# Kernel tuning notes

Measured on AMD Instinct MI355X. Metric: run time of the kernel, lower is better.

Reference implementation:

```python
import jax, jax.numpy as jnp
import numpy as np

# DynamicMaskHead config (CondLaneHead defaults, head_layers=3, channels=64)
N, INS_PER_IMG, C, H, W = 4, 8, 64, 160, 256
CIN = C + 2  # coords concatenated
L1, L2, L3 = (C + 2) * C, C * C, C * 1  # weight_nums = [4224, 4096, 64]
B1, B2, B3 = C, C, 1                     # bias_nums   = [64, 64, 1]
NUM_PARAMS = L1 + L2 + L3 + B1 + B2 + B3  # 8513
MASK_BIAS_SHIFT = 2.19  # subtracted from last bias when is_mask=True


def setup_inputs() -> dict:
    key = jax.random.key(0)
    k1, k2 = jax.random.split(key)
    x = jax.random.normal(k1, (N, C, H, W), dtype=jnp.float32)
    mask_head_params = jax.random.normal(k2, (N * INS_PER_IMG, NUM_PARAMS), dtype=jnp.float32) * 0.05
    num_ins = np.full((N,), INS_PER_IMG, dtype=np.int32)  # static per-image instance counts
    return {"x": x, "mask_head_params": mask_head_params, "num_ins": num_ins}


def _locations(h, w, dtype):
    # compute_locations with stride=1: +stride//2 == +0; original normalization
    # (locations[:0], locations[:1]) is a no-op slice, so coords stay unnormalized.
    loc_x = jnp.broadcast_to(jnp.arange(w, dtype=dtype)[None, :], (h, w))
    loc_y = jnp.broadcast_to(jnp.arange(h, dtype=dtype)[:, None], (h, w))
    return jnp.stack([loc_x, loc_y], axis=0)  # [2, H, W]


def reference(x, mask_head_params, num_ins):
    n, _, h, w = x.shape
    loc = _locations(h, w, x.dtype)
    xa = jnp.concatenate([jnp.broadcast_to(loc[None], (n, 2, h, w)), x], axis=1)  # [N, 66, H, W]

    # replicate each image's features per instance (grouped-conv input)
    img_idx = np.repeat(np.arange(n), np.asarray(num_ins))  # static
    num_insts = img_idx.shape[0]
    feats = xa[img_idx].reshape(num_insts, CIN, h * w)  # [I, 66, L]

    # parse_dynamic_params: split flat params into per-instance 1x1 conv weights/biases
    splits = jnp.split(mask_head_params, np.cumsum([L1, L2, L3, B1, B2]), axis=1)
    w0 = splits[0].reshape(num_insts, C, CIN)
    w1 = splits[1].reshape(num_insts, C, C)
    w2 = splits[2].reshape(num_insts, 1, C)
    b0 = splits[3]
    b1 = splits[4]
    b2 = splits[5] - MASK_BIAS_SHIFT  # is_mask=True

    # grouped 1x1 convs == per-instance small matmuls (batched GEMM)
    hdn = jax.nn.relu(jnp.einsum('ioc,icl->iol', w0, feats) + b0[:, :, None])
    hdn = jax.nn.relu(jnp.einsum('ioc,icl->iol', w1, hdn) + b1[:, :, None])
    out = jnp.einsum('ioc,icl->iol', w2, hdn) + b2[:, :, None]  # [I, 1, L]
    return out.reshape(1, num_insts, h, w)
```

## Files before the change

kernel.cpp:

```cpp
#include <hip/hip_runtime.h>
#include <hip/hip_bf16.h>


#define NP 8513
#define HW 40960
#define ISTRIDE 18432
#define OFF_VECA 8192
#define OFF_W1 9216
#define OFF_VECB 17408

typedef __attribute__((ext_vector_type(8))) short bf16x8;
typedef __attribute__((ext_vector_type(4))) float f32x4;
typedef __attribute__((ext_vector_type(2))) unsigned uint2v;

__device__ inline unsigned short f2bf(float f) {
  union { float f; unsigned u; } v; v.f = f;
  unsigned r = v.u + 0x7fffu + ((v.u >> 16) & 1u);
  return (unsigned short)(r >> 16);
}
__device__ inline unsigned pk2(float a, float b) {
  __hip_bfloat162 h = __float22bfloat162_rn(float2{a, b});
  union { __hip_bfloat162 h; unsigned u; } v; v.h = h;
  return v.u;
}
__device__ inline void gld16(const void* g, void* l) {
  __builtin_amdgcn_global_load_lds(
      (const __attribute__((address_space(1))) unsigned*)g,
      (__attribute__((address_space(3))) unsigned*)l, 16, 0, 0);
}

__global__ void condlane_prep(const float* __restrict__ params,
                              char* __restrict__ ws) {
  const int inst = blockIdx.x >> 3, part = blockIdx.x & 7;
  const float* __restrict__ p = params + inst * NP;
  char* base = ws + inst * ISTRIDE;
  const int t = threadIdx.x;
  if (part < 4) {
    unsigned short* dst = (unsigned short*)base;
#pragma unroll
    for (int it = 0; it < 4; it++) {
      const int e = (part * 4 + it) * 256 + t;
      const int frag = e >> 9, lane = (e >> 3) & 63, j = e & 7;
      const int m = (frag >> 1) * 16 + (lane & 15);
      const int k = (frag & 1) * 32 + ((lane >> 4) << 3) + j;
      dst[e] = f2bf(p[m * 66 + 2 + k]);
    }
  } else {
    unsigned short* dst = (unsigned short*)(base + OFF_W1);
#pragma unroll
    for (int it = 0; it < 4; it++) {
      const int e = ((part - 4) * 4 + it) * 256 + t;
      const int frag = e >> 9, lane = (e >> 3) & 63, j = e & 7;
      const int m = (frag >> 1) * 16 + (lane & 15);
      const int k = (frag & 1) * 32 + ((lane >> 4) << 3) + j;
      dst[e] = f2bf(p[4224 + m * 64 + k]);
    }
    if (part == 4) {
      float* vA = (float*)(base + OFF_VECA);
      float* vB = (float*)(base + OFF_VECB);
      if (t < 64) {
        vA[t]       = p[8384 + t];
        vA[64 + t]  = p[t * 66];
        vA[128 + t] = p[t * 66 + 1];
        vB[t]       = p[8448 + t];
        vB[64 + t]  = p[8320 + t];
      } else if (t == 64) vB[128] = p[8512] - 2.19f;
    }
  }
}

__global__ __launch_bounds__(256, 3) void condlane_main(
    const float* __restrict__ x, const char* __restrict__ ws,
    float* __restrict__ out) {
  __shared__ __align__(16) char smem[2 * ISTRIDE];
  const int img = blockIdx.y, row = blockIdx.x;
  const int tid = threadIdx.x, lane = tid & 63, wave = tid >> 6;
  const int col = lane & 15, q = lane >> 4;
  const char* const wsb = ws + img * 8 * ISTRIDE;

  auto dma = [&](int i, char* buf) {
    const char* src = wsb + i * ISTRIDE;
#pragma unroll
    for (int u = 0; u < 4; u++) {
      const int off = (wave * 4 + u) * 1024;
      gld16(src + off + lane * 16, buf + off);
    }
    if (wave < 2) {
      const int off = (16 + wave) * 1024;
      gld16(src + off + lane * 16, buf + off);
    }
  };
  dma(0, smem);

  bf16x8 bfr[4][2];
  {
    const float* gx = x + img * 64 * HW + row * 256 + wave * 64;
#pragma unroll
    for (int nt = 0; nt < 4; nt++)
#pragma unroll
      for (int ks = 0; ks < 2; ks++) {
        float f[8];
#pragma unroll
        for (int j = 0; j < 8; j++)
          f[j] = gx[(ks * 32 + q * 8 + j) * HW + nt * 16 + col];
        union { bf16x8 v; unsigned d[4]; } u;
#pragma unroll
        for (int jj = 0; jj < 4; jj++) u.d[jj] = pk2(f[2 * jj], f[2 * jj + 1]);
        bfr[nt][ks] = u.v;
      }
  }
  __syncthreads();

  const float fyv = (float)row;
  float fxv[4];
#pragma unroll
  for (int nt = 0; nt < 4; nt++) fxv[nt] = (float)(wave * 64 + nt * 16 + col);
  float* const outb = out + img * 8 * HW + row * 256 + wave * 64;

  for (int i = 0; i < 8; i++) {
    char* const wb = smem + (i & 1) * ISTRIDE;
    if (i < 7) dma(i + 1, smem + ((i + 1) & 1) * ISTRIDE);
    const float* const vecA = (const float*)(wb + OFF_VECA);
    const float* const vecB = (const float*)(wb + OFF_VECB);

    f32x4 acc[4][4];
#pragma unroll
    for (int mt = 0; mt < 4; mt++) {
      const int ro = mt * 16 + q * 4;
      const f32x4 b0v = *(const f32x4*)(vecA + ro);
      const f32x4 wxv = *(const f32x4*)(vecA + 64 + ro);
      const f32x4 wyv = *(const f32x4*)(vecA + 128 + ro);
      const f32x4 byv = b0v + wyv * fyv;
#pragma unroll
      for (int nt = 0; nt < 4; nt++) acc[mt][nt] = byv + wxv * fxv[nt];
    }
#pragma unroll
    for (int mt = 0; mt < 4; mt++) {
      const bf16x8 a0 = *(const bf16x8*)(wb + (mt * 2 + 0) * 1024 + lane * 16);
      const bf16x8 a1 = *(const bf16x8*)(wb + (mt * 2 + 1) * 1024 + lane * 16);
#pragma unroll
      for (int nt = 0; nt < 4; nt++) {
        f32x4 c = __builtin_amdgcn_mfma_f32_16x16x32_bf16(a0, bfr[nt][0],
                                                          acc[mt][nt], 0, 0, 0);
        acc[mt][nt] = __builtin_amdgcn_mfma_f32_16x16x32_bf16(a1, bfr[nt][1],
                                                              c, 0, 0, 0);
      }
    }

    bf16x8 hbf[4][2];
#pragma unroll
    for (int nt = 0; nt < 4; nt++) {
      unsigned pd[4][2];
#pragma unroll
      for (int mt = 0; mt < 4; mt++) {
        const f32x4 v = acc[mt][nt];
        pd[mt][0] = pk2(fmaxf(v.x, 0.f), fmaxf(v.y, 0.f));
        pd[mt][1] = pk2(fmaxf(v.z, 0.f), fmaxf(v.w, 0.f));
      }
#pragma unroll
      for (int ks = 0; ks < 2; ks++) {
        uint2v r0 = __builtin_amdgcn_permlane32_swap(
            pd[2 * ks][0], pd[2 * ks + 1][0], false, false);
        uint2v s0 = __builtin_amdgcn_permlane16_swap(r0[0], r0[1], false, false);
        uint2v r1 = __builtin_amdgcn_permlane32_swap(
            pd[2 * ks][1], pd[2 * ks + 1][1], false, false);
        uint2v s1 = __builtin_amdgcn_permlane16_swap(r1[0], r1[1], false, false);
        union { unsigned d[4]; bf16x8 v; } u;
        u.d[0] = s0[0];
        u.d[1] = s1[0];
        u.d[2] = s0[1];
        u.d[3] = s1[1];
        hbf[nt][ks] = u.v;
      }
    }

    float s[4] = {0.f, 0.f, 0.f, 0.f};
#pragma unroll
    for (int mt = 0; mt < 4; mt++) {
      const bf16x8 a0 = *(const bf16x8*)(wb + OFF_W1 + (mt * 2 + 0) * 1024 + lane * 16);
      const bf16x8 a1 = *(const bf16x8*)(wb + OFF_W1 + (mt * 2 + 1) * 1024 + lane * 16);
      const int ro = mt * 16 + q * 4;
      const f32x4 cb  = *(const f32x4*)(vecB + ro);
      const f32x4 w2v = *(const f32x4*)(vecB + 64 + ro);
#pragma unroll
      for (int nt = 0; nt < 4; nt++) {
        f32x4 c = __builtin_amdgcn_mfma_f32_16x16x32_bf16(a0, hbf[nt][0], cb, 0, 0, 0);
        const f32x4 v = __builtin_amdgcn_mfma_f32_16x16x32_bf16(a1, hbf[nt][1], c, 0, 0, 0);
        s[nt] += w2v.x * fmaxf(v.x, 0.f) + w2v.y * fmaxf(v.y, 0.f) +
                 w2v.z * fmaxf(v.z, 0.f) + w2v.w * fmaxf(v.w, 0.f);
      }
    }
    const float b2i = vecB[128];

#pragma unroll
    for (int nt = 0; nt < 4; nt++) {
      float r = s[nt];
      r += __shfl_xor(r, 16, 64);
      r += __shfl_xor(r, 32, 64);
      if (lane < 16) outb[i * HW + nt * 16 + col] = r + b2i;
    }

    if (i < 7) __syncthreads();
  }
}

extern "C" void kernel_launch(void* const* d_in, const int* in_sizes, int n_in,
                              void* d_out, int out_size, void* d_ws, size_t ws_size,
                              hipStream_t stream) {
  const float* x      = (const float*)d_in[0];
  const float* params = (const float*)d_in[1];
  float* out = (float*)d_out;

  condlane_prep<<<256, 256, 0, stream>>>(params, (char*)d_ws);
  condlane_main<<<dim3(160, 4), 256, 0, stream>>>(x, (const char*)d_ws, out);
}
```

Baseline: 122.3 us.

## Split work across four times more blocks: half-rows and half the instances per block

Each block now covers 128 pixels (half a row) and 4 of the 8 instances, with a 3D grid of 320x4x2, so the grid has four times as many blocks. Per-thread register state shrinks (fewer accumulator tiles), and launch bounds rise to 4 blocks per CU to improve occupancy and fill more CUs. The cost is that each x tile is loaded twice (once per instance half), weights are DMA'd for more blocks, and each block does less work to amortise setup.

```diff
diff --git a/kernel.cpp b/kernel.cpp
--- a/kernel.cpp
+++ b/kernel.cpp
@@ -69,14 +69,14 @@
   }
 }
 
-__global__ __launch_bounds__(256, 3) void condlane_main(
+__global__ __launch_bounds__(256, 4) void condlane_main(
     const float* __restrict__ x, const char* __restrict__ ws,
     float* __restrict__ out) {
   __shared__ __align__(16) char smem[2 * ISTRIDE];
-  const int img = blockIdx.y, row = blockIdx.x;
+  const int img = blockIdx.y, bx = blockIdx.x, zi = blockIdx.z;
   const int tid = threadIdx.x, lane = tid & 63, wave = tid >> 6;
   const int col = lane & 15, q = lane >> 4;
-  const char* const wsb = ws + img * 8 * ISTRIDE;
+  const char* const wsb = ws + (img * 8 + zi * 4) * ISTRIDE;
 
   auto dma = [&](int i, char* buf) {
     const char* src = wsb + i * ISTRIDE;
@@ -92,11 +92,11 @@
   };
   dma(0, smem);
 
-  bf16x8 bfr[4][2];
+  bf16x8 bfr[2][2];
   {
-    const float* gx = x + img * 64 * HW + row * 256 + wave * 64;
-#pragma unroll
-    for (int nt = 0; nt < 4; nt++)
+    const float* gx = x + img * 64 * HW + bx * 128 + wave * 32;
+#pragma unroll
+    for (int nt = 0; nt < 2; nt++)
 #pragma unroll
       for (int ks = 0; ks < 2; ks++) {
         float f[8];
@@ -111,19 +111,18 @@
   }
   __syncthreads();
 
-  const float fyv = (float)row;
-  float fxv[4];
-#pragma unroll
-  for (int nt = 0; nt < 4; nt++) fxv[nt] = (float)(wave * 64 + nt * 16 + col);
-  float* const outb = out + img * 8 * HW + row * 256 + wave * 64;
-
-  for (int i = 0; i < 8; i++) {
+  const float fyv = (float)(bx >> 1);
+  const float fx0 = (float)((bx & 1) * 128 + wave * 32 + col);
+  float* const outb = out + (img * 8 + zi * 4) * HW + bx * 128 + wave * 32;
+
+#pragma unroll 1
+  for (int i = 0; i < 4; i++) {
     char* const wb = smem + (i & 1) * ISTRIDE;
-    if (i < 7) dma(i + 1, smem + ((i + 1) & 1) * ISTRIDE);
+    if (i < 3) dma(i + 1, smem + ((i + 1) & 1) * ISTRIDE);
     const float* const vecA = (const float*)(wb + OFF_VECA);
     const float* const vecB = (const float*)(wb + OFF_VECB);
 
-    f32x4 acc[4][4];
+    f32x4 acc[4][2];
 #pragma unroll
     for (int mt = 0; mt < 4; mt++) {
       const int ro = mt * 16 + q * 4;
@@ -131,15 +130,15 @@
       const f32x4 wxv = *(const f32x4*)(vecA + 64 + ro);
       const f32x4 wyv = *(const f32x4*)(vecA + 128 + ro);
       const f32x4 byv = b0v + wyv * fyv;
-#pragma unroll
-      for (int nt = 0; nt < 4; nt++) acc[mt][nt] = byv + wxv * fxv[nt];
+      acc[mt][0] = byv + wxv * fx0;
+      acc[mt][1] = byv + wxv * (fx0 + 16.0f);
     }
 #pragma unroll
     for (int mt = 0; mt < 4; mt++) {
       const bf16x8 a0 = *(const bf16x8*)(wb + (mt * 2 + 0) * 1024 + lane * 16);
       const bf16x8 a1 = *(const bf16x8*)(wb + (mt * 2 + 1) * 1024 + lane * 16);
 #pragma unroll
-      for (int nt = 0; nt < 4; nt++) {
+      for (int nt = 0; nt < 2; nt++) {
         f32x4 c = __builtin_amdgcn_mfma_f32_16x16x32_bf16(a0, bfr[nt][0],
                                                           acc[mt][nt], 0, 0, 0);
         acc[mt][nt] = __builtin_amdgcn_mfma_f32_16x16x32_bf16(a1, bfr[nt][1],
@@ -147,9 +146,9 @@
       }
     }
 
-    bf16x8 hbf[4][2];
-#pragma unroll
-    for (int nt = 0; nt < 4; nt++) {
+    bf16x8 hbf[2][2];
+#pragma unroll
+    for (int nt = 0; nt < 2; nt++) {
       unsigned pd[4][2];
 #pragma unroll
       for (int mt = 0; mt < 4; mt++) {
@@ -174,7 +173,7 @@
       }
     }
 
-    float s[4] = {0.f, 0.f, 0.f, 0.f};
+    float s0 = 0.f, s1 = 0.f;
 #pragma unroll
     for (int mt = 0; mt < 4; mt++) {
       const bf16x8 a0 = *(const bf16x8*)(wb + OFF_W1 + (mt * 2 + 0) * 1024 + lane * 16);
@@ -182,25 +181,23 @@
       const int ro = mt * 16 + q * 4;
       const f32x4 cb  = *(const f32x4*)(vecB + ro);
       const f32x4 w2v = *(const f32x4*)(vecB + 64 + ro);
-#pragma unroll
-      for (int nt = 0; nt < 4; nt++) {
-        f32x4 c = __builtin_amdgcn_mfma_f32_16x16x32_bf16(a0, hbf[nt][0], cb, 0, 0, 0);
-        const f32x4 v = __builtin_amdgcn_mfma_f32_16x16x32_bf16(a1, hbf[nt][1], c, 0, 0, 0);
-        s[nt] += w2v.x * fmaxf(v.x, 0.f) + w2v.y * fmaxf(v.y, 0.f) +
-                 w2v.z * fmaxf(v.z, 0.f) + w2v.w * fmaxf(v.w, 0.f);
-      }
+      f32x4 c0 = __builtin_amdgcn_mfma_f32_16x16x32_bf16(a0, hbf[0][0], cb, 0, 0, 0);
+      const f32x4 v0 = __builtin_amdgcn_mfma_f32_16x16x32_bf16(a1, hbf[0][1], c0, 0, 0, 0);
+      f32x4 c1 = __builtin_amdgcn_mfma_f32_16x16x32_bf16(a0, hbf[1][0], cb, 0, 0, 0);
+      const f32x4 v1 = __builtin_amdgcn_mfma_f32_16x16x32_bf16(a1, hbf[1][1], c1, 0, 0, 0);
+      s0 += w2v.x * fmaxf(v0.x, 0.f) + w2v.y * fmaxf(v0.y, 0.f) +
+            w2v.z * fmaxf(v0.z, 0.f) + w2v.w * fmaxf(v0.w, 0.f);
+      s1 += w2v.x * fmaxf(v1.x, 0.f) + w2v.y * fmaxf(v1.y, 0.f) +
+            w2v.z * fmaxf(v1.z, 0.f) + w2v.w * fmaxf(v1.w, 0.f);
     }
     const float b2i = vecB[128];
 
-#pragma unroll
-    for (int nt = 0; nt < 4; nt++) {
-      float r = s[nt];
-      r += __shfl_xor(r, 16, 64);
-      r += __shfl_xor(r, 32, 64);
-      if (lane < 16) outb[i * HW + nt * 16 + col] = r + b2i;
-    }
-
-    if (i < 7) __syncthreads();
+    s0 += __shfl_xor(s0, 16, 64); s0 += __shfl_xor(s0, 32, 64);
+    s1 += __shfl_xor(s1, 16, 64); s1 += __shfl_xor(s1, 32, 64);
+    if (lane < 32)
+      outb[i * HW + q * 16 + col] = (q ? s1 : s0) + b2i;
+
+    if (i < 3) __syncthreads();
   }
 }
 
@@ -212,5 +209,5 @@
   float* out = (float*)d_out;
 
   condlane_prep<<<256, 256, 0, stream>>>(params, (char*)d_ws);
-  condlane_main<<<dim3(160, 4), 256, 0, stream>>>(x, (const char*)d_ws, out);
-}
+  condlane_main<<<dim3(320, 4, 2), 256, 0, stream>>>(x, (const char*)d_ws, out);
+}
```

Result: faster. 116.3 us (-4.9%).
